# Kernel tuning notes

Hardware: AMD Instinct MI355X
Metric: run time of the kernel (lower is better)

Reference implementation:

```python
import jax, jax.numpy as jnp
import numpy as np

B, S, T = 256, 1024, 64

def setup_inputs() -> dict:
    key = jax.random.key(0)
    k1, k2, k3, k4, k5 = jax.random.split(key, 5)
    emissions = jax.random.normal(k1, (B, S, T), dtype=jnp.float32)
    tags = jax.random.randint(k2, (B, S), 0, T, dtype=jnp.int64)
    mask = jnp.ones((B, S), dtype=jnp.int32)
    transitions = jax.random.normal(k3, (T, T), dtype=jnp.float32) * 0.1
    start_transitions = jax.random.normal(k4, (T,), dtype=jnp.float32) * 0.1
    end_transitions = jax.random.normal(k5, (T,), dtype=jnp.float32) * 0.1
    return {"emissions": emissions, "tags": tags, "mask": mask,
            "transitions": transitions, "start_transitions": start_transitions,
            "end_transitions": end_transitions}


def _gold_score(emissions, tags, maskf, transitions, start_transitions, end_transitions):
    # emission score at each gold tag: [B, S]
    emit = jnp.take_along_axis(emissions, tags[:, :, None], axis=2)[:, :, 0]
    # transition score between consecutive gold tags: [B, S-1]
    trans = transitions[tags[:, :-1], tags[:, 1:]]
    score = start_transitions[tags[:, 0]] + emit[:, 0]
    score = score + jnp.sum((trans + emit[:, 1:]) * maskf[:, 1:], axis=1)
    last_pos = maskf.astype(jnp.int32).sum(axis=1) - 1           # [B]
    last_tags = jnp.take_along_axis(tags, last_pos[:, None], axis=1)[:, 0]
    return score + end_transitions[last_tags]


def _log_partition(emissions, maskf, transitions, start_transitions, end_transitions):
    alpha0 = start_transitions[None, :] + emissions[:, 0]        # [B, T]

    def step(alpha, xs):
        emit_t, m_t = xs                                         # [B, T], [B]
        # scores[b, i, j] = alpha[b, i] + transitions[i, j] + emit_t[b, j]
        scores = alpha[:, :, None] + transitions[None, :, :] + emit_t[:, None, :]
        new_alpha = jax.nn.logsumexp(scores, axis=1)             # [B, T]
        alpha = jnp.where(m_t[:, None] > 0, new_alpha, alpha)
        return alpha, None

    xs = (jnp.swapaxes(emissions[:, 1:], 0, 1), jnp.swapaxes(maskf[:, 1:], 0, 1))
    alpha, _ = jax.lax.scan(step, alpha0, xs)
    return jax.nn.logsumexp(alpha + end_transitions[None, :], axis=1)  # [B]


def reference(emissions, tags, mask, transitions, start_transitions, end_transitions):
    maskf = mask.astype(emissions.dtype)
    log_Z = _log_partition(emissions, maskf, transitions, start_transitions, end_transitions)
    score = _gold_score(emissions, tags, maskf, transitions, start_transitions, end_transitions)
    return jnp.mean(log_Z - score)
```

## Files before the change

kernel.cpp:

```cpp
#include <hip/hip_runtime.h>

#define Bn 256
#define Sn 1024
#define Tn 64
#define NCH 16
#define BURN 64
#define SLAB 4
#define RAWSTR 260
#define CROW 72
#define MROW 129
#define LN2 0.69314718055994531f
#define L7LN2 4.8520302639196169f

typedef __attribute__((ext_vector_type(8))) short short8;
typedef __attribute__((ext_vector_type(4))) float f32x4;

__device__ __forceinline__ unsigned short f2bf_rne(float f) {
  unsigned u = __float_as_uint(f);
  u = (u + 0x7fffu + ((u >> 16) & 1u)) >> 16;
  return (unsigned short)u;
}
__device__ __forceinline__ unsigned pk2(float hi, float lo) {
  return __builtin_amdgcn_perm(__float_as_uint(hi), __float_as_uint(lo), 0x07060302);
}
__device__ __forceinline__ unsigned pke(float a, float b) {
  return (unsigned)f2bf_rne(__expf(a - L7LN2)) |
         ((unsigned)f2bf_rne(__expf(b - L7LN2)) << 16);
}
__device__ __forceinline__ short8 cat4(uint2 a, uint2 b) {
  union { unsigned u[4]; short8 s; } x;
  x.u[0] = a.x; x.u[1] = a.y; x.u[2] = b.x; x.u[3] = b.y;
  return x.s;
}
__device__ __forceinline__ void gl_lds16(const void* src, void* dst) {
  __builtin_amdgcn_global_load_lds(
      (const __attribute__((address_space(1))) void*)src,
      (__attribute__((address_space(3))) void*)dst, 16, 0, 0);
}
__device__ __forceinline__ void gl_lds4(const void* src, void* dst) {
  __builtin_amdgcn_global_load_lds(
      (const __attribute__((address_space(1))) void*)src,
      (__attribute__((address_space(3))) void*)dst, 4, 0, 0);
}

__global__ __launch_bounds__(128, 1) void crf_scan(
    const float* __restrict__ em, const int* __restrict__ tags,
    const int* __restrict__ mask, const float* __restrict__ trans,
    const float* __restrict__ startt, const float* __restrict__ endt,
    float* __restrict__ wsL, float* __restrict__ wsGold,
    int* __restrict__ wsM, float* __restrict__ wsSE, float* __restrict__ wsA,
    int* __restrict__ cnt, float* __restrict__ out) {
  const int g = blockIdx.x & 15;
  const int c = blockIdx.x >> 4;
  const int Wc = (c == 0) ? 0 : BURN;
  const int Lc = (c == NCH - 1) ? 63 : 64;
  const int TOT = Wc + Lc;
  const int NSLAB = (TOT + SLAB - 1) / SLAB;
  const int t0 = 64 * c + 1;
  const int tstart = t0 - Wc;
  const int tid = threadIdx.x;
  const int wid = tid >> 6;
  const int lane = tid & 63;
  const int m = lane & 15;
  const int q = lane >> 4;
  const int mrow = 8 * (m >> 2) + (m & 3);

  __shared__ __align__(16) float rawS[2][16 * RAWSTR];
  __shared__ __align__(16) short convS[2][SLAB * 16 * CROW];
  __shared__ int maskL[16 * MROW];
  __shared__ int lastF;
  __shared__ float eend[64];
  __shared__ float rsum[2];

  short8 a00, a01, a10, a11, a20, a21, a30, a31;
  uint2 st0, st1, st2, st3;
  float Slog = 0.f;
  int K = 0, NL = 0;
  const f32x4 zero4 = {0.f, 0.f, 0.f, 0.f};

  auto issue_slab = [&](int s) {
    if (s >= NSLAB) return;
    float* dstb = rawS[s & 1];
    const int rem = TOT - 4 * s;
    if (rem >= SLAB) {
      for (int mm = 0; mm < 16; ++mm)
        gl_lds16(em + ((size_t)(16 * g + mm) * Sn + tstart + 4 * s) * 64 + lane * 4,
                 dstb + mm * RAWSTR);
    } else {
      for (int mm = 0; mm < 16; ++mm)
        for (int u = 0; u < rem; ++u)
          gl_lds4(em + ((size_t)(16 * g + mm) * Sn + tstart + 4 * s + u) * 64 + lane,
                  dstb + mm * RAWSTR + u * 64);
    }
  };
  auto convert_slab = [&](int s) {
    if (s >= NSLAB) return;
    const int mm = lane & 15, seg = lane >> 4;
    const float* rp = rawS[s & 1] + mm * RAWSTR + seg * 16;
    short* cb = convS[s & 1];
    const int vu = min(SLAB, TOT - 4 * s);
    const int base = (seg >> 1) * 32 + (seg & 1) * 8;
    for (int u = 0; u < vu; ++u) {
      float4 v0 = *(const float4*)(rp + u * 64 + 0);
      float4 v1 = *(const float4*)(rp + u * 64 + 4);
      float4 v2 = *(const float4*)(rp + u * 64 + 8);
      float4 v3 = *(const float4*)(rp + u * 64 + 12);
      uint4 o0, o1;
      o0.x = pke(v0.x, v0.y); o0.y = pke(v0.z, v0.w);
      o1.x = pke(v1.x, v1.y); o1.y = pke(v1.z, v1.w);
      o0.z = pke(v2.x, v2.y); o0.w = pke(v2.z, v2.w);
      o1.z = pke(v3.x, v3.y); o1.w = pke(v3.z, v3.w);
      short* cw = cb + (u * 16 + mm) * CROW + base;
      *(uint4*)(cw) = o0;
      *(uint4*)(cw + 16) = o1;
    }
  };

  if (wid == 0) {
#define LOADA(tm, kc, dst) { \
    _Pragma("unroll") for (int jj = 0; jj < 8; ++jj) { \
      int kk = kc * 32 + q * 8 + jj; \
      dst[jj] = (short)f2bf_rne(__expf(trans[kk * Tn + (32 * ((tm) >> 1) + 4 * ((tm) & 1) + mrow)])); \
    } }
    LOADA(0, 0, a00) LOADA(0, 1, a01) LOADA(1, 0, a10) LOADA(1, 1, a11)
    LOADA(2, 0, a20) LOADA(2, 1, a21) LOADA(3, 0, a30) LOADA(3, 1, a31)
#undef LOADA
    if (c == 0) {
#define INIT0(off, ss) { \
      float4 sv = *(const float4*)(startt + (off)); \
      float4 ev = *(const float4*)(em + (size_t)(16 * g + m) * Sn * Tn + (off)); \
      ss.x = (unsigned)f2bf_rne(__expf(sv.x + ev.x)) | \
             ((unsigned)f2bf_rne(__expf(sv.y + ev.y)) << 16); \
      ss.y = (unsigned)f2bf_rne(__expf(sv.z + ev.z)) | \
             ((unsigned)f2bf_rne(__expf(sv.w + ev.w)) << 16); }
      INIT0(8 * q, st0) INIT0(8 * q + 4, st1)
      INIT0(32 + 8 * q, st2) INIT0(36 + 8 * q, st3)
#undef INIT0
    } else {
      st0.x = 0x3F803F80u; st0.y = 0x3F803F80u; st1 = st0; st2 = st0; st3 = st0;
    }
    issue_slab(0);
  } else {
    for (int mm = 0; mm < 16; ++mm) {
      gl_lds4(mask + (size_t)(16 * g + mm) * Sn + tstart + lane,
              (void*)(maskL + mm * MROW));
      bool special = (c == NCH - 1) && (g == 15) && (mm == 15);
      if (!special)
        gl_lds4(mask + (size_t)(16 * g + mm) * Sn + tstart + 64 + lane,
                (void*)(maskL + mm * MROW + 64));
    }
    {
      const int bm = 16 * g + m;
      const int qq = q;
      const int* tg = tags + (size_t)bm * Sn;
      const int* mkb = mask + (size_t)bm * Sn;
      const float* emb = em + (size_t)bm * Sn * Tn;
      float acc = 0.f;
      int cntg = 0;
      #pragma unroll 4
      for (int i = 0; i < 16; ++i) {
        int t = t0 + qq + 4 * i;
        bool ok = t < t0 + Lc;
        int ts = ok ? t : t0;
        int mv = mkb[ts];
        int tp = tg[ts - 1], tc = tg[ts];
        float w = trans[tp * Tn + tc] + emb[(size_t)ts * Tn + tc];
        acc += (ok && mv) ? w : 0.f;
        cntg += ok ? mv : 0;
      }
      acc += __shfl_xor(acc, 16); acc += __shfl_xor(acc, 32);
      cntg += __shfl_xor(cntg, 16); cntg += __shfl_xor(cntg, 32);
      if (qq == 0) { wsGold[c * 256 + bm] = acc; wsM[c * 256 + bm] = cntg; }
    }
    if (c == NCH - 1 && g == 15) {
      int t = tstart + 64 + lane;
      if (t < Sn) maskL[15 * MROW + 64 + lane] = mask[(size_t)255 * Sn + t];
    }
  }
  asm volatile("s_waitcnt vmcnt(0)" ::: "memory");
  __syncthreads();

  if (wid == 0) issue_slab(1);
  else convert_slab(0);
  asm volatile("s_waitcnt vmcnt(0)" ::: "memory");
  __syncthreads();

#define UNP(ss, x0, x1, x2, x3) \
  x0 = __uint_as_float(ss.x << 16); x1 = __uint_as_float(ss.x & 0xffff0000u); \
  x2 = __uint_as_float(ss.y << 16); x3 = __uint_as_float(ss.y & 0xffff0000u);

  for (int r = 0; r < NSLAB; ++r) {
    if (wid == 0) {
      issue_slab(r + 2);
      const short* cbase = convS[r & 1];
      #pragma unroll
      for (int u = 0; u < SLAB; ++u) {
        const int tt = 4 * r + u;
        if (tt < TOT) {
          if (((r & 1) == 0) && u == 0) {
            float x00, x01, x02, x03, x10, x11, x12, x13;
            float x20, x21, x22, x23, x30, x31, x32, x33;
            UNP(st0, x00, x01, x02, x03) UNP(st1, x10, x11, x12, x13)
            UNP(st2, x20, x21, x22, x23) UNP(st3, x30, x31, x32, x33)
            float sm = (((x00 + x01) + (x02 + x03)) + ((x10 + x11) + (x12 + x13)))
                     + (((x20 + x21) + (x22 + x23)) + ((x30 + x31) + (x32 + x33)));
            sm += __shfl_xor(sm, 16); sm += __shfl_xor(sm, 32);
            if (c != 0 && tt == BURN) { Slog = __logf(sm); K = 0; NL = 0; }
            int k = 127 - (int)((__float_as_uint(sm) >> 23) & 255u);
            float fk = __uint_as_float((unsigned)(127 + k) << 23);
            x00 *= fk; x01 *= fk; x02 *= fk; x03 *= fk;
            x10 *= fk; x11 *= fk; x12 *= fk; x13 *= fk;
            x20 *= fk; x21 *= fk; x22 *= fk; x23 *= fk;
            x30 *= fk; x31 *= fk; x32 *= fk; x33 *= fk;
            st0.x = pk2(x01, x00); st0.y = pk2(x03, x02);
            st1.x = pk2(x11, x10); st1.y = pk2(x13, x12);
            st2.x = pk2(x21, x20); st2.y = pk2(x23, x22);
            st3.x = pk2(x31, x30); st3.y = pk2(x33, x32);
            K += k;
          }
          const short* ep = cbase + (u * 16 + m) * CROW;
          uint2 eu0 = *(const uint2*)(ep + 0 + 4 * q);
          uint2 eu1 = *(const uint2*)(ep + 16 + 4 * q);
          uint2 eu2 = *(const uint2*)(ep + 32 + 4 * q);
          uint2 eu3 = *(const uint2*)(ep + 48 + 4 * q);
          int mv = maskL[m * MROW + tt];
          short8 b0 = cat4(st0, st1);
          short8 b1 = cat4(st2, st3);
          f32x4 d0 = __builtin_amdgcn_mfma_f32_16x16x32_bf16(a00, b0, zero4, 0, 0, 0);
          f32x4 d1 = __builtin_amdgcn_mfma_f32_16x16x32_bf16(a10, b0, zero4, 0, 0, 0);
          f32x4 d2 = __builtin_amdgcn_mfma_f32_16x16x32_bf16(a20, b0, zero4, 0, 0, 0);
          f32x4 d3 = __builtin_amdgcn_mfma_f32_16x16x32_bf16(a30, b0, zero4, 0, 0, 0);
          d0 = __builtin_amdgcn_mfma_f32_16x16x32_bf16(a01, b1, d0, 0, 0, 0);
          d1 = __builtin_amdgcn_mfma_f32_16x16x32_bf16(a11, b1, d1, 0, 0, 0);
          d2 = __builtin_amdgcn_mfma_f32_16x16x32_bf16(a21, b1, d2, 0, 0, 0);
          d3 = __builtin_amdgcn_mfma_f32_16x16x32_bf16(a31, b1, d3, 0, 0, 0);
          const bool live = (mv != 0);
#define EPI(dd, eu, ss) { \
          float e0 = __uint_as_float(eu.x << 16); \
          float e1 = __uint_as_float(eu.x & 0xffff0000u); \
          float e2 = __uint_as_float(eu.y << 16); \
          float e3 = __uint_as_float(eu.y & 0xffff0000u); \
          unsigned nx = pk2(dd[1] * e1, dd[0] * e0); \
          unsigned ny = pk2(dd[3] * e3, dd[2] * e2); \
          ss.x = live ? nx : ss.x; \
          ss.y = live ? ny : ss.y; }
          EPI(d0, eu0, st0) EPI(d1, eu1, st1) EPI(d2, eu2, st2) EPI(d3, eu3, st3)
#undef EPI
          NL += (live && tt >= Wc) ? 1 : 0;
        }
      }
    } else {
      convert_slab(r + 1);
    }
    asm volatile("s_waitcnt vmcnt(0)" ::: "memory");
    __syncthreads();
  }

  if (wid == 0) {
    float x00, x01, x02, x03, x10, x11, x12, x13;
    float x20, x21, x22, x23, x30, x31, x32, x33;
    UNP(st0, x00, x01, x02, x03) UNP(st1, x10, x11, x12, x13)
    UNP(st2, x20, x21, x22, x23) UNP(st3, x30, x31, x32, x33)
    float sm = (((x00 + x01) + (x02 + x03)) + ((x10 + x11) + (x12 + x13)))
             + (((x20 + x21) + (x22 + x23)) + ((x30 + x31) + (x32 + x33)));
    sm += __shfl_xor(sm, 16); sm += __shfl_xor(sm, 32);
    const int bm = 16 * g + m;
    float L = __logf(sm) - Slog + LN2 * (float)(7 * NL - K);
    if (q == 0) wsL[c * 256 + bm] = L;
    if (c == NCH - 1) {
      if (q == 0) wsSE[bm] = __logf(sm);
      wsA[(8 * q + 0) * 256 + bm] = x00;  wsA[(8 * q + 1) * 256 + bm] = x01;
      wsA[(8 * q + 2) * 256 + bm] = x02;  wsA[(8 * q + 3) * 256 + bm] = x03;
      wsA[(8 * q + 4) * 256 + bm] = x10;  wsA[(8 * q + 5) * 256 + bm] = x11;
      wsA[(8 * q + 6) * 256 + bm] = x12;  wsA[(8 * q + 7) * 256 + bm] = x13;
      wsA[(32 + 8 * q + 0) * 256 + bm] = x20; wsA[(32 + 8 * q + 1) * 256 + bm] = x21;
      wsA[(32 + 8 * q + 2) * 256 + bm] = x22; wsA[(32 + 8 * q + 3) * 256 + bm] = x23;
      wsA[(36 + 8 * q + 0) * 256 + bm] = x30; wsA[(36 + 8 * q + 1) * 256 + bm] = x31;
      wsA[(36 + 8 * q + 2) * 256 + bm] = x32; wsA[(36 + 8 * q + 3) * 256 + bm] = x33;
    }
  }
#undef UNP

  __threadfence();
  __syncthreads();
  if (tid == 0) lastF = (atomicAdd(cnt, 1) == 255) ? 1 : 0;
  __syncthreads();
  if (lastF) {
    __threadfence();
    if (tid < 64) eend[tid] = __expf(endt[tid]);
    __syncthreads();
    float vsum = 0.f;
    for (int bb = tid; bb < Bn; bb += 128) {
      float sumL = 0.f, gold = 0.f;
      int msum = 0;
      #pragma unroll
      for (int cc = 0; cc < NCH; ++cc) {
        sumL += wsL[cc * 256 + bb];
        gold += wsGold[cc * 256 + bb];
        msum += wsM[cc * 256 + bb];
      }
      msum += mask[(size_t)bb * Sn];
      float se = 0.f;
      for (int jj = 0; jj < Tn; ++jj) se += wsA[jj * 256 + bb] * eend[jj];
      float logZ = sumL + __logf(se) - wsSE[bb];
      int tg0 = tags[(size_t)bb * Sn];
      int lastTag = tags[(size_t)bb * Sn + (msum - 1)];
      gold += startt[tg0] + em[(size_t)bb * Sn * Tn + tg0] + endt[lastTag];
      vsum += logZ - gold;
    }
    #pragma unroll
    for (int o = 32; o > 0; o >>= 1) vsum += __shfl_xor(vsum, o, 64);
    if (lane == 0) rsum[wid] = vsum;
    __syncthreads();
    if (tid == 0) out[0] = (rsum[0] + rsum[1]) * (1.0f / Bn);
  }
}

extern "C" void kernel_launch(void* const* d_in, const int* in_sizes, int n_in,
                              void* d_out, int out_size, void* d_ws, size_t ws_size,
                              hipStream_t stream) {
  const float* em     = (const float*)d_in[0];
  const int*   tags   = (const int*)d_in[1];
  const int*   mask   = (const int*)d_in[2];
  const float* trans  = (const float*)d_in[3];
  const float* startt = (const float*)d_in[4];
  const float* endt   = (const float*)d_in[5];
  float* out = (float*)d_out;

  float* wsL    = (float*)d_ws;
  float* wsGold = wsL + NCH * 256;
  int*   wsM    = (int*)(wsGold + NCH * 256);
  float* wsSE   = (float*)(wsM + NCH * 256);
  float* wsA    = wsSE + 256;
  int*   cnt    = (int*)(wsA + 64 * 256);

  hipMemsetAsync(cnt, 0, sizeof(int), stream);
  crf_scan<<<256, 128, 0, stream>>>(em, tags, mask, trans, startt, endt,
                                    wsL, wsGold, wsM, wsSE, wsA, cnt, out);
}
```

Before: 166.3 us.

## Triple-buffer raw emission slabs and relax per-slab waits to partial vmcnt

Adds a third raw staging buffer so global-to-LDS loads run three slabs ahead instead of two, and the loader wave waits only for the oldest slab (vmcnt(16)) rather than draining all outstanding loads each iteration. The full barrier plus drain is replaced by a raw s_barrier with per-wave waitcnt, and the scan and convert loops are split into full and tail variants so the common case has no per-step bounds check. The aim is to keep memory latency off the serial MFMA scan's critical path. In exchange it uses more LDS, which may lower occupancy, and the hand-counted vmcnt depends on each slab issuing exactly 16 loads.

```diff
diff --git a/kernel.cpp b/kernel.cpp
--- a/kernel.cpp
+++ b/kernel.cpp
@@ -65,7 +65,7 @@
   const int q = lane >> 4;
   const int mrow = 8 * (m >> 2) + (m & 3);
 
-  __shared__ __align__(16) float rawS[2][16 * RAWSTR];
+  __shared__ __align__(16) float rawS[3][16 * RAWSTR];
   __shared__ __align__(16) short convS[2][SLAB * 16 * CROW];
   __shared__ int maskL[16 * MROW];
   __shared__ int lastF;
@@ -80,7 +80,7 @@
 
   auto issue_slab = [&](int s) {
     if (s >= NSLAB) return;
-    float* dstb = rawS[s & 1];
+    float* dstb = rawS[s % 3];
     const int rem = TOT - 4 * s;
     if (rem >= SLAB) {
       for (int mm = 0; mm < 16; ++mm)
@@ -93,27 +93,36 @@
                   dstb + mm * RAWSTR + u * 64);
     }
   };
-  auto convert_slab = [&](int s) {
+  auto conv_u = [&](const float* rp, short* cb, int mm, int base, int u) {
+    float4 v0 = *(const float4*)(rp + u * 64 + 0);
+    float4 v1 = *(const float4*)(rp + u * 64 + 4);
+    float4 v2 = *(const float4*)(rp + u * 64 + 8);
+    float4 v3 = *(const float4*)(rp + u * 64 + 12);
+    uint4 o0, o1;
+    o0.x = pke(v0.x, v0.y); o0.y = pke(v0.z, v0.w);
+    o1.x = pke(v1.x, v1.y); o1.y = pke(v1.z, v1.w);
+    o0.z = pke(v2.x, v2.y); o0.w = pke(v2.z, v2.w);
+    o1.z = pke(v3.x, v3.y); o1.w = pke(v3.z, v3.w);
+    short* cw = cb + (u * 16 + mm) * CROW + base;
+    *(uint4*)(cw) = o0;
+    *(uint4*)(cw + 16) = o1;
+  };
+  auto convert_full = [&](int s) {
+    const int mm = lane & 15, seg = lane >> 4;
+    const float* rp = rawS[s % 3] + mm * RAWSTR + seg * 16;
+    short* cb = convS[s & 1];
+    const int base = (seg >> 1) * 32 + (seg & 1) * 8;
+    #pragma unroll
+    for (int u = 0; u < SLAB; ++u) conv_u(rp, cb, mm, base, u);
+  };
+  auto convert_tail = [&](int s) {
     if (s >= NSLAB) return;
     const int mm = lane & 15, seg = lane >> 4;
-    const float* rp = rawS[s & 1] + mm * RAWSTR + seg * 16;
+    const float* rp = rawS[s % 3] + mm * RAWSTR + seg * 16;
     short* cb = convS[s & 1];
+    const int base = (seg >> 1) * 32 + (seg & 1) * 8;
     const int vu = min(SLAB, TOT - 4 * s);
-    const int base = (seg >> 1) * 32 + (seg & 1) * 8;
-    for (int u = 0; u < vu; ++u) {
-      float4 v0 = *(const float4*)(rp + u * 64 + 0);
-      float4 v1 = *(const float4*)(rp + u * 64 + 4);
-      float4 v2 = *(const float4*)(rp + u * 64 + 8);
-      float4 v3 = *(const float4*)(rp + u * 64 + 12);
-      uint4 o0, o1;
-      o0.x = pke(v0.x, v0.y); o0.y = pke(v0.z, v0.w);
-      o1.x = pke(v1.x, v1.y); o1.y = pke(v1.z, v1.w);
-      o0.z = pke(v2.x, v2.y); o0.w = pke(v2.z, v2.w);
-      o1.z = pke(v3.x, v3.y); o1.w = pke(v3.z, v3.w);
-      short* cw = cb + (u * 16 + mm) * CROW + base;
-      *(uint4*)(cw) = o0;
-      *(uint4*)(cw + 16) = o1;
-    }
+    for (int u = 0; u < vu; ++u) conv_u(rp, cb, mm, base, u);
   };
 
   if (wid == 0) {
@@ -140,6 +149,8 @@
       st0.x = 0x3F803F80u; st0.y = 0x3F803F80u; st1 = st0; st2 = st0; st3 = st0;
     }
     issue_slab(0);
+    issue_slab(1);
+    asm volatile("s_waitcnt vmcnt(0)" ::: "memory");
   } else {
     for (int mm = 0; mm < 16; ++mm) {
       gl_lds4(mask + (size_t)(16 * g + mm) * Sn + tstart + lane,
@@ -176,84 +187,101 @@
       int t = tstart + 64 + lane;
       if (t < Sn) maskL[15 * MROW + 64 + lane] = mask[(size_t)255 * Sn + t];
     }
-  }
-  asm volatile("s_waitcnt vmcnt(0)" ::: "memory");
+    asm volatile("s_waitcnt vmcnt(0) lgkmcnt(0)" ::: "memory");
+  }
   __syncthreads();
 
-  if (wid == 0) issue_slab(1);
-  else convert_slab(0);
-  asm volatile("s_waitcnt vmcnt(0)" ::: "memory");
+  if (wid == 0) {
+    issue_slab(2);
+    asm volatile("s_waitcnt vmcnt(0)" ::: "memory");
+  } else {
+    convert_full(0);
+    asm volatile("s_waitcnt lgkmcnt(0)" ::: "memory");
+  }
   __syncthreads();
 
 #define UNP(ss, x0, x1, x2, x3) \
   x0 = __uint_as_float(ss.x << 16); x1 = __uint_as_float(ss.x & 0xffff0000u); \
   x2 = __uint_as_float(ss.y << 16); x3 = __uint_as_float(ss.y & 0xffff0000u);
 
+  auto renorm = [&](int ttz) {
+    float x00, x01, x02, x03, x10, x11, x12, x13;
+    float x20, x21, x22, x23, x30, x31, x32, x33;
+    UNP(st0, x00, x01, x02, x03) UNP(st1, x10, x11, x12, x13)
+    UNP(st2, x20, x21, x22, x23) UNP(st3, x30, x31, x32, x33)
+    float sm = (((x00 + x01) + (x02 + x03)) + ((x10 + x11) + (x12 + x13)))
+             + (((x20 + x21) + (x22 + x23)) + ((x30 + x31) + (x32 + x33)));
+    sm += __shfl_xor(sm, 16); sm += __shfl_xor(sm, 32);
+    if (c != 0 && ttz == BURN) { Slog = __logf(sm); K = 0; NL = 0; }
+    int k = 127 - (int)((__float_as_uint(sm) >> 23) & 255u);
+    float fk = __uint_as_float((unsigned)(127 + k) << 23);
+    x00 *= fk; x01 *= fk; x02 *= fk; x03 *= fk;
+    x10 *= fk; x11 *= fk; x12 *= fk; x13 *= fk;
+    x20 *= fk; x21 *= fk; x22 *= fk; x23 *= fk;
+    x30 *= fk; x31 *= fk; x32 *= fk; x33 *= fk;
+    st0.x = pk2(x01, x00); st0.y = pk2(x03, x02);
+    st1.x = pk2(x11, x10); st1.y = pk2(x13, x12);
+    st2.x = pk2(x21, x20); st2.y = pk2(x23, x22);
+    st3.x = pk2(x31, x30); st3.y = pk2(x33, x32);
+    K += k;
+  };
+
+  auto scan_step = [&](const short* ep, int tt) {
+    uint2 eu0 = *(const uint2*)(ep + 0 + 4 * q);
+    uint2 eu1 = *(const uint2*)(ep + 16 + 4 * q);
+    uint2 eu2 = *(const uint2*)(ep + 32 + 4 * q);
+    uint2 eu3 = *(const uint2*)(ep + 48 + 4 * q);
+    int mv = maskL[m * MROW + tt];
+    short8 b0 = cat4(st0, st1);
+    short8 b1 = cat4(st2, st3);
+    f32x4 d0 = __builtin_amdgcn_mfma_f32_16x16x32_bf16(a00, b0, zero4, 0, 0, 0);
+    f32x4 d1 = __builtin_amdgcn_mfma_f32_16x16x32_bf16(a10, b0, zero4, 0, 0, 0);
+    f32x4 d2 = __builtin_amdgcn_mfma_f32_16x16x32_bf16(a20, b0, zero4, 0, 0, 0);
+    f32x4 d3 = __builtin_amdgcn_mfma_f32_16x16x32_bf16(a30, b0, zero4, 0, 0, 0);
+    d0 = __builtin_amdgcn_mfma_f32_16x16x32_bf16(a01, b1, d0, 0, 0, 0);
+    d1 = __builtin_amdgcn_mfma_f32_16x16x32_bf16(a11, b1, d1, 0, 0, 0);
+    d2 = __builtin_amdgcn_mfma_f32_16x16x32_bf16(a21, b1, d2, 0, 0, 0);
+    d3 = __builtin_amdgcn_mfma_f32_16x16x32_bf16(a31, b1, d3, 0, 0, 0);
+    const bool live = (mv != 0);
+#define EPI(dd, eu, ss) { \
+    float e0 = __uint_as_float(eu.x << 16); \
+    float e1 = __uint_as_float(eu.x & 0xffff0000u); \
+    float e2 = __uint_as_float(eu.y << 16); \
+    float e3 = __uint_as_float(eu.y & 0xffff0000u); \
+    unsigned nx = pk2(dd[1] * e1, dd[0] * e0); \
+    unsigned ny = pk2(dd[3] * e3, dd[2] * e2); \
+    ss.x = live ? nx : ss.x; \
+    ss.y = live ? ny : ss.y; }
+    EPI(d0, eu0, st0) EPI(d1, eu1, st1) EPI(d2, eu2, st2) EPI(d3, eu3, st3)
+#undef EPI
+    NL += (live && tt >= Wc) ? 1 : 0;
+  };
+
+  const int RT = (TOT - 4) >> 2;
   for (int r = 0; r < NSLAB; ++r) {
     if (wid == 0) {
-      issue_slab(r + 2);
+      issue_slab(r + 3);
+      if ((r & 1) == 0) renorm(4 * r);
       const short* cbase = convS[r & 1];
-      #pragma unroll
-      for (int u = 0; u < SLAB; ++u) {
-        const int tt = 4 * r + u;
-        if (tt < TOT) {
-          if (((r & 1) == 0) && u == 0) {
-            float x00, x01, x02, x03, x10, x11, x12, x13;
-            float x20, x21, x22, x23, x30, x31, x32, x33;
-            UNP(st0, x00, x01, x02, x03) UNP(st1, x10, x11, x12, x13)
-            UNP(st2, x20, x21, x22, x23) UNP(st3, x30, x31, x32, x33)
-            float sm = (((x00 + x01) + (x02 + x03)) + ((x10 + x11) + (x12 + x13)))
-                     + (((x20 + x21) + (x22 + x23)) + ((x30 + x31) + (x32 + x33)));
-            sm += __shfl_xor(sm, 16); sm += __shfl_xor(sm, 32);
-            if (c != 0 && tt == BURN) { Slog = __logf(sm); K = 0; NL = 0; }
-            int k = 127 - (int)((__float_as_uint(sm) >> 23) & 255u);
-            float fk = __uint_as_float((unsigned)(127 + k) << 23);
-            x00 *= fk; x01 *= fk; x02 *= fk; x03 *= fk;
-            x10 *= fk; x11 *= fk; x12 *= fk; x13 *= fk;
-            x20 *= fk; x21 *= fk; x22 *= fk; x23 *= fk;
-            x30 *= fk; x31 *= fk; x32 *= fk; x33 *= fk;
-            st0.x = pk2(x01, x00); st0.y = pk2(x03, x02);
-            st1.x = pk2(x11, x10); st1.y = pk2(x13, x12);
-            st2.x = pk2(x21, x20); st2.y = pk2(x23, x22);
-            st3.x = pk2(x31, x30); st3.y = pk2(x33, x32);
-            K += k;
-          }
-          const short* ep = cbase + (u * 16 + m) * CROW;
-          uint2 eu0 = *(const uint2*)(ep + 0 + 4 * q);
-          uint2 eu1 = *(const uint2*)(ep + 16 + 4 * q);
-          uint2 eu2 = *(const uint2*)(ep + 32 + 4 * q);
-          uint2 eu3 = *(const uint2*)(ep + 48 + 4 * q);
-          int mv = maskL[m * MROW + tt];
-          short8 b0 = cat4(st0, st1);
-          short8 b1 = cat4(st2, st3);
-          f32x4 d0 = __builtin_amdgcn_mfma_f32_16x16x32_bf16(a00, b0, zero4, 0, 0, 0);
-          f32x4 d1 = __builtin_amdgcn_mfma_f32_16x16x32_bf16(a10, b0, zero4, 0, 0, 0);
-          f32x4 d2 = __builtin_amdgcn_mfma_f32_16x16x32_bf16(a20, b0, zero4, 0, 0, 0);
-          f32x4 d3 = __builtin_amdgcn_mfma_f32_16x16x32_bf16(a30, b0, zero4, 0, 0, 0);
-          d0 = __builtin_amdgcn_mfma_f32_16x16x32_bf16(a01, b1, d0, 0, 0, 0);
-          d1 = __builtin_amdgcn_mfma_f32_16x16x32_bf16(a11, b1, d1, 0, 0, 0);
-          d2 = __builtin_amdgcn_mfma_f32_16x16x32_bf16(a21, b1, d2, 0, 0, 0);
-          d3 = __builtin_amdgcn_mfma_f32_16x16x32_bf16(a31, b1, d3, 0, 0, 0);
-          const bool live = (mv != 0);
-#define EPI(dd, eu, ss) { \
-          float e0 = __uint_as_float(eu.x << 16); \
-          float e1 = __uint_as_float(eu.x & 0xffff0000u); \
-          float e2 = __uint_as_float(eu.y << 16); \
-          float e3 = __uint_as_float(eu.y & 0xffff0000u); \
-          unsigned nx = pk2(dd[1] * e1, dd[0] * e0); \
-          unsigned ny = pk2(dd[3] * e3, dd[2] * e2); \
-          ss.x = live ? nx : ss.x; \
-          ss.y = live ? ny : ss.y; }
-          EPI(d0, eu0, st0) EPI(d1, eu1, st1) EPI(d2, eu2, st2) EPI(d3, eu3, st3)
-#undef EPI
-          NL += (live && tt >= Wc) ? 1 : 0;
-        }
+      if (r < RT) {
+        #pragma unroll
+        for (int u = 0; u < SLAB; ++u)
+          scan_step(cbase + (u * 16 + m) * CROW, 4 * r + u);
+      } else {
+        #pragma unroll
+        for (int u = 0; u < SLAB; ++u)
+          if (4 * r + u < TOT)
+            scan_step(cbase + (u * 16 + m) * CROW, 4 * r + u);
       }
+      if (r + 3 < NSLAB) asm volatile("s_waitcnt vmcnt(16)" ::: "memory");
+      else               asm volatile("s_waitcnt vmcnt(0)" ::: "memory");
     } else {
-      convert_slab(r + 1);
-    }
-    asm volatile("s_waitcnt vmcnt(0)" ::: "memory");
-    __syncthreads();
+      if (r < RT) convert_full(r + 1);
+      else        convert_tail(r + 1);
+      asm volatile("s_waitcnt lgkmcnt(0)" ::: "memory");
+    }
+    __builtin_amdgcn_s_barrier();
+    asm volatile("" ::: "memory");
   }
 
   if (wid == 0) {
```

Result: no change. 169.5 us (+1.9%).
